# Kernel tuning notes

Hardware: AMD Instinct MI355X
Metric: run time of the kernel (lower is better)

The kernel has to match this reference:

```python
import jax, jax.numpy as jnp
import numpy as np

N = 11          # neighborhood size
HEADS = 4
DIM = 128
OUT_DIM = 128
HEAD_DIM = DIM // HEADS
LN_EPS = 1e-5


def unfold_neighborhood(x, n=N):
    # x: [B,H,W,C] -> [B,H,W,N,N,C]; matches torch F.unfold semantics:
    # out[b,h,w,i,j,c] = padded[b, h+i, w+j, c]
    B, H, W, C = x.shape
    P = (n - 1) // 2
    xp = jnp.pad(x, ((0, 0), (P, P), (P, P), (0, 0)))
    patches = jnp.stack(
        [xp[:, i:i + H, j:j + W, :] for i in range(n) for j in range(n)],
        axis=3)  # [B,H,W,N*N,C]
    return patches.reshape(B, H, W, n, n, C)


def setup_inputs() -> dict:
    key = jax.random.key(0)
    ks = jax.random.split(key, 6)
    B, H, W = 2, 64, 64
    q = jax.random.normal(ks[0], (B, H, W, DIM), dtype=jnp.float32)
    kv = jax.random.normal(ks[1], (B, H, W, DIM), dtype=jnp.float32)
    pos_enc = jax.random.normal(ks[2], (N, N, DIM), dtype=jnp.float32)
    # mlp: Linear(N*N*heads -> out_dim)
    fan_in = N * N * HEADS
    bound = 1.0 / np.sqrt(fan_in)
    mlp_w = jax.random.uniform(ks[3], (fan_in, OUT_DIM), jnp.float32, -bound, bound)
    mlp_b = jax.random.uniform(ks[4], (OUT_DIM,), jnp.float32, -bound, bound)
    ln_g = jnp.ones((OUT_DIM,), jnp.float32)
    ln_b = jnp.zeros((OUT_DIM,), jnp.float32)
    return {"q": q, "kv": kv, "pos_enc": pos_enc, "mlp_w": mlp_w,
            "mlp_b": mlp_b, "ln_g": ln_g, "ln_b": ln_b}


def reference(q, kv, pos_enc, mlp_w, mlp_b, ln_g, ln_b):
    B, H, W, C = q.shape
    kv_n = unfold_neighborhood(kv, N) + pos_enc            # [B,H,W,N,N,C]
    # faithful raw row-major reinterpretation of (N,N,C) -> (heads, N^2, head_dim)
    kv_mh = kv_n.reshape(B, H, W, HEADS, N * N, HEAD_DIM)
    q_mh = q.reshape(B, H, W, HEADS, HEAD_DIM)
    # per-pixel per-head dot products (note: original never applies scale)
    scores = jnp.einsum('bxyhnd,bxyhd->bxyhn', kv_mh, q_mh)
    scores = scores.reshape(B, H, W, HEADS * N * N)        # [B,H,W,484]
    mlp_out = jax.nn.gelu(scores @ mlp_w + mlp_b, approximate=False)
    # short_cut is Identity since dim == out_dim
    x = q + mlp_out
    mu = jnp.mean(x, axis=-1, keepdims=True)
    var = jnp.mean(jnp.square(x - mu), axis=-1, keepdims=True)
    return (x - mu) * jax.lax.rsqrt(var + LN_EPS) * ln_g + ln_b
```

## Files before the change

kernel.cpp:

```cpp
#include <hip/hip_runtime.h>
#include <math.h>

#define NB 11
#define PAD 5
#define DIM 128
#define NN 121
#define S_TOT 484
#define IMG 64
#define TILE 8
#define PDIM 74
#define SCP 520
#define PSCP 488
#define UCOLS 18
#define UCELLS 198
#define NT_KV 50
#define NT_POS 31
#define NPAD (2 * PDIM * PDIM)
#define KVB ((NPAD + 3) / 4)
#define LN_EPS 1e-5f

typedef __attribute__((ext_vector_type(8))) short bf16x8;
typedef __attribute__((ext_vector_type(4))) float f32x4;

static __device__ __forceinline__ unsigned short f2bf(float f) {
    unsigned u = __float_as_uint(f);
    u += 0x7FFF + ((u >> 16) & 1);
    return (unsigned short)(u >> 16);
}

__global__ __launch_bounds__(256) void prep_kernel(
    const float* __restrict__ kv, const float* __restrict__ w,
    const float* __restrict__ pos, unsigned short* __restrict__ pkvb,
    unsigned short* __restrict__ wfrag, unsigned short* __restrict__ posB)
{
    const int blk  = blockIdx.x;
    const int lane = threadIdx.x & 63;
    const int sub  = threadIdx.x >> 6;
    if (blk < KVB) {
        const int row = blk * 4 + sub;
        if (row < NPAD) {
            const int b  = row / (PDIM * PDIM);
            const int rr = row - b * PDIM * PDIM;
            const int py = rr / PDIM;
            const int px = rr - py * PDIM;
            const int ky = py - PAD, kx = px - PAD;
            unsigned v = 0;
            if ((unsigned)ky < (unsigned)IMG && (unsigned)kx < (unsigned)IMG) {
                const float2 f = *(const float2*)(kv + (((size_t)b * IMG + ky) * IMG + kx) * DIM + 2 * lane);
                v = (unsigned)f2bf(f.x) | ((unsigned)f2bf(f.y) << 16);
            }
            *(unsigned*)(pkvb + (size_t)row * DIM + 2 * lane) = v;
        }
    } else if (blk < KVB + 32) {
        const int idx = (blk - KVB) * 4 + sub;
        const int t   = idx & 15;
        const int n   = ((idx >> 4) << 4) + (lane & 15);
        const int kb  = t * 32 + ((lane >> 4) << 3);
        unsigned short v[8];
        #pragma unroll
        for (int j = 0; j < 8; ++j) {
            const int k = kb + j;
            v[j] = (k < S_TOT) ? f2bf(w[(size_t)k * DIM + n]) : (unsigned short)0;
        }
        *(uint4*)(wfrag + (((size_t)idx * 64 + lane) << 3)) = *(const uint4*)v;
    } else {
        const int nt = (blk - KVB - 32) * 4 + sub;
        if (nt < NT_POS) {
            const int m    = lane & 15, quad = lane >> 4;
            const int p    = 4 * nt + (m >> 2);
            const int r    = m & 3;
            unsigned short v[8];
            #pragma unroll
            for (int j = 0; j < 8; ++j)
                v[j] = (p <= 120) ? f2bf(pos[(size_t)p * DIM + 32 * r + 8 * quad + j])
                                  : (unsigned short)0;
            *(uint4*)(posB + (((size_t)nt * 64 + lane) << 3)) = *(const uint4*)v;
        }
    }
}

__global__ __launch_bounds__(512) void nca_kernel(
    const float* __restrict__ q, const unsigned short* __restrict__ pkvb,
    const unsigned short* __restrict__ posB, const unsigned short* __restrict__ wfrag,
    const float* __restrict__ bias, const float* __restrict__ gam,
    const float* __restrict__ bet, float* __restrict__ out)
{
    const int tile = blockIdx.x;
    const int pix0 = tile * TILE;
    const int x0 = pix0 & 63;
    const int y  = (pix0 >> 6) & 63;
    const int b  = pix0 >> 12;
    const int tid = threadIdx.x;

    __shared__ float qs[TILE][DIM];
    __shared__ float psc[TILE][PSCP];
    __shared__ __align__(16) unsigned short sc_bf[TILE][SCP];
    __shared__ float mlp[TILE][DIM];

    for (int i = tid; i < TILE * DIM; i += 512)
        qs[i >> 7][i & 127] = q[(size_t)pix0 * DIM + i];
    for (int i = tid; i < TILE * (SCP - S_TOT); i += 512)
        sc_bf[i / (SCP - S_TOT)][S_TOT + i % (SCP - S_TOT)] = 0;

    {
        const int wid  = tid >> 6;
        const int lane = tid & 63;
        const int n    = lane & 15, quad = lane >> 4;
        const int mt   = wid & 1;
        const int w4   = wid >> 1;
        const int pxl  = 4 * mt + quad;

        const float* qa = q + ((size_t)(pix0 + 4 * mt + (n >> 2))) * DIM
                            + 32 * (n & 3) + 8 * quad;
        const float4 fa0 = *(const float4*)qa;
        const float4 fa1 = *(const float4*)(qa + 4);
        unsigned short aq_[8] = {f2bf(fa0.x), f2bf(fa0.y), f2bf(fa0.z), f2bf(fa0.w),
                                 f2bf(fa1.x), f2bf(fa1.y), f2bf(fa1.z), f2bf(fa1.w)};
        const bf16x8 Aq = *(const bf16x8*)aq_;

        {
            const unsigned short* pb = posB + ((size_t)lane << 3);
            int nt = w4;
            bf16x8 Bc = *(const bf16x8*)(pb + (size_t)nt * 512);
            while (nt < NT_POS) {
                const int ntn = nt + 4;
                bf16x8 Bn = Bc;
                if (ntn < NT_POS) Bn = *(const bf16x8*)(pb + (size_t)ntn * 512);
                f32x4 acc = {0.f, 0.f, 0.f, 0.f};
                acc = __builtin_amdgcn_mfma_f32_16x16x32_bf16(Aq, Bc, acc, 0, 0, 0);
                const int s = 16 * nt + n;
                if (s < S_TOT) {
                    const int h = (271 * s) >> 15;
                    const float v = (h == 0) ? acc[0] : (h == 1) ? acc[1]
                                  : (h == 2) ? acc[2] : acc[3];
                    psc[pxl][s] = v;
                }
                Bc = Bn; nt = ntn;
            }
        }
        __syncthreads();

        {
            const int r  = n & 3;
            const int co = 32 * r + 8 * quad;
            const unsigned short* kvb = pkvb
                + ((size_t)((b * PDIM + y) * PDIM) + x0) * DIM + co;
            int c = 4 * w4 + (n >> 2);
            int i = 0, u = c;
            int nt = w4;
            bf16x8 Bc = *(const bf16x8*)(kvb + (size_t)(i * PDIM + u) * DIM);
            while (nt < NT_KV) {
                int cn = c + 16, in_ = i, un = u + 16;
                if (un >= UCOLS) { un -= UCOLS; ++in_; }
                if (cn > UCELLS - 1) { in_ = 10; un = UCOLS - 1; }
                bf16x8 Bn = Bc;
                if (nt + 4 < NT_KV)
                    Bn = *(const bf16x8*)(kvb + (size_t)(in_ * PDIM + un) * DIM);
                f32x4 acc = {0.f, 0.f, 0.f, 0.f};
                acc = __builtin_amdgcn_mfma_f32_16x16x32_bf16(Aq, Bc, acc, 0, 0, 0);
                const int jr = u - pxl;
                if ((unsigned)jr < 11u) {
                    const int s = 44 * i + 4 * jr + r;
                    const int h = (271 * s) >> 15;
                    const float v = ((h == 0) ? acc[0] : (h == 1) ? acc[1]
                                   : (h == 2) ? acc[2] : acc[3]) + psc[pxl][s];
                    sc_bf[pxl][s] = f2bf(v);
                }
                Bc = Bn; c = cn; i = in_; u = un; nt += 4;
            }
        }
    }
    __syncthreads();

    {
        const int wv   = tid >> 6;
        const int lane = tid & 63;
        const int m    = lane & 15;
        const int quad = lane >> 4;
        const unsigned short* bfr = wfrag + (((size_t)(wv * 16) * 64 + lane) << 3);
        const unsigned short* ap  = &sc_bf[m & 7][quad * 8];
        f32x4 acc = {0.f, 0.f, 0.f, 0.f};
        bf16x8 b0 = *(const bf16x8*)(bfr);
        bf16x8 b1 = *(const bf16x8*)(bfr + 512);
        bf16x8 b2 = *(const bf16x8*)(bfr + 1024);
        bf16x8 b3 = *(const bf16x8*)(bfr + 1536);
        #pragma unroll
        for (int t = 0; t < 16; ++t) {
            const bf16x8 a = *(const bf16x8*)(ap + t * 32);
            bf16x8 bn = b3;
            if (t + 4 < 16) bn = *(const bf16x8*)(bfr + (t + 4) * 512);
            acc = __builtin_amdgcn_mfma_f32_16x16x32_bf16(a, b0, acc, 0, 0, 0);
            b0 = b1; b1 = b2; b2 = b3; b3 = bn;
        }
        if (quad < 2) {
            #pragma unroll
            for (int reg = 0; reg < 4; ++reg)
                mlp[quad * 4 + reg][wv * 16 + m] = acc[reg];
        }
    }
    __syncthreads();

    for (int idx = tid; idx < TILE * DIM; idx += 512) {
        const int pix = idx >> 7, cc = idx & 127;
        const float v = mlp[pix][cc] + bias[cc];
        const float gl = 0.5f * v * (1.f + erff(v * 0.70710678118654752f));
        qs[pix][cc] += gl;
    }
    __syncthreads();

    {
        const int lane = tid & 63, wid = tid >> 6;
        const float v0 = qs[wid][lane], v1 = qs[wid][lane + 64];
        float sum = v0 + v1;
        #pragma unroll
        for (int off = 1; off < 64; off <<= 1) sum += __shfl_xor(sum, off, 64);
        const float mean = sum * (1.f / 128.f);
        const float d0 = v0 - mean, d1 = v1 - mean;
        float sq = d0 * d0 + d1 * d1;
        #pragma unroll
        for (int off = 1; off < 64; off <<= 1) sq += __shfl_xor(sq, off, 64);
        const float rstd = rsqrtf(sq * (1.f / 128.f) + LN_EPS);
        float* op = out + (size_t)(pix0 + wid) * DIM;
        op[lane]      = d0 * rstd * gam[lane]      + bet[lane];
        op[lane + 64] = d1 * rstd * gam[lane + 64] + bet[lane + 64];
    }
}

__global__ __launch_bounds__(512) void nca_kernel_nopad(
    const float* __restrict__ q, const float* __restrict__ kvsrc,
    const float* __restrict__ pos, const float* __restrict__ w,
    const float* __restrict__ bias, const float* __restrict__ gam,
    const float* __restrict__ bet, float* __restrict__ out)
{
    const int tile = blockIdx.x;
    const int pix0 = tile * TILE;
    const int x0 = pix0 & 63;
    const int y  = (pix0 >> 6) & 63;
    const int b  = pix0 >> 12;
    const int tid = threadIdx.x;

    __shared__ float qs[TILE][DIM];
    __shared__ float sc[S_TOT][TILE];
    __shared__ float part[4][TILE][DIM];

    for (int i = tid; i < TILE * DIM; i += 512)
        qs[i >> 7][i & 127] = q[(size_t)pix0 * DIM + i];
    __syncthreads();

    {
        const int pix = tid >> 6;
        const int grp = (tid >> 4) & 3;
        const int l16 = tid & 15;
        const int r   = l16 >> 2;
        const int dq  = 8 * (l16 & 3);
        const int ch  = 8 * l16;
        const int xpix = x0 + pix;
        int p = grp, i = 0, j = grp;
        int h = 0, rem = 4 * grp + r;
        const float* kvb  = kvsrc + (size_t)b * IMG * IMG * DIM + ch;
        const float* posb = pos + ch;
        float4 q0 = *(const float4*)(&qs[pix][dq]);
        float4 q1 = *(const float4*)(&qs[pix][dq + 4]);
        for (int it = 0; it < 31; ++it) {
            if (p <= 120) {
                float4 k0 = make_float4(0.f,0.f,0.f,0.f), k1 = k0;
                const int ky = y + i - PAD, kx = xpix + j - PAD;
                if (((unsigned)ky < (unsigned)IMG) && ((unsigned)kx < (unsigned)IMG)) {
                    const float* kp = kvb + (size_t)(ky * IMG + kx) * DIM;
                    k0 = *(const float4*)(kp);
                    k1 = *(const float4*)(kp + 4);
                }
                const float4 p0 = *(const float4*)(posb + (size_t)p * DIM);
                const float4 p1 = *(const float4*)(posb + (size_t)p * DIM + 4);
                float t = (k0.x + p0.x) * q0.x + (k0.y + p0.y) * q0.y
                        + (k0.z + p0.z) * q0.z + (k0.w + p0.w) * q0.w
                        + (k1.x + p1.x) * q1.x + (k1.y + p1.y) * q1.y
                        + (k1.z + p1.z) * q1.z + (k1.w + p1.w) * q1.w;
                t += __shfl_xor(t, 1, 64);
                t += __shfl_xor(t, 2, 64);
                if ((l16 & 3) == 0) sc[4 * p + r][pix] = t;
            }
            p += 4; j += 4;
            if (j >= NB) { j -= NB; ++i; }
            rem += 16;
            if (rem >= NN) {
                rem -= NN; ++h;
                q0 = *(const float4*)(&qs[pix][h * 32 + dq]);
                q1 = *(const float4*)(&qs[pix][h * 32 + dq + 4]);
            }
        }
    }
    __syncthreads();

    {
        const int l  = tid & 63;
        const int wv = tid >> 6;
        const int g  = wv >> 1;
        const int ph = wv & 1;
        const float* wc  = w + (size_t)(g * NN) * DIM + l;
        const float* scp = &sc[g * NN][ph * 4];
        float a00=0,a01=0,a10=0,a11=0,a20=0,a21=0,a30=0,a31=0;
        #pragma unroll 2
        for (int s = 0; s < NN; ++s) {
            const float4 sv = *(const float4*)(scp + s * 8);
            const float w0 = wc[(size_t)s * DIM];
            const float w1 = wc[(size_t)s * DIM + 64];
            a00 += sv.x * w0; a01 += sv.x * w1;
            a10 += sv.y * w0; a11 += sv.y * w1;
            a20 += sv.z * w0; a21 += sv.z * w1;
            a30 += sv.w * w0; a31 += sv.w * w1;
        }
        const int pb = ph * 4;
        part[g][pb+0][l] = a00; part[g][pb+0][l+64] = a01;
        part[g][pb+1][l] = a10; part[g][pb+1][l+64] = a11;
        part[g][pb+2][l] = a20; part[g][pb+2][l+64] = a21;
        part[g][pb+3][l] = a30; part[g][pb+3][l+64] = a31;
    }
    __syncthreads();

    for (int idx = tid; idx < TILE * DIM; idx += 512) {
        const int pix = idx >> 7, cc = idx & 127;
        float v = part[0][pix][cc] + part[1][pix][cc]
                + part[2][pix][cc] + part[3][pix][cc] + bias[cc];
        const float gl = 0.5f * v * (1.f + erff(v * 0.70710678118654752f));
        qs[pix][cc] += gl;
    }
    __syncthreads();

    {
        const int lane = tid & 63, wid = tid >> 6;
        const float v0 = qs[wid][lane], v1 = qs[wid][lane + 64];
        float sum = v0 + v1;
        #pragma unroll
        for (int off = 1; off < 64; off <<= 1) sum += __shfl_xor(sum, off, 64);
        const float mean = sum * (1.f / 128.f);
        const float d0 = v0 - mean, d1 = v1 - mean;
        float sq = d0 * d0 + d1 * d1;
        #pragma unroll
        for (int off = 1; off < 64; off <<= 1) sq += __shfl_xor(sq, off, 64);
        const float rstd = rsqrtf(sq * (1.f / 128.f) + LN_EPS);
        float* op = out + (size_t)(pix0 + wid) * DIM;
        op[lane]      = d0 * rstd * gam[lane]      + bet[lane];
        op[lane + 64] = d1 * rstd * gam[lane + 64] + bet[lane + 64];
    }
}

extern "C" void kernel_launch(void* const* d_in, const int* in_sizes, int n_in,
                              void* d_out, int out_size, void* d_ws, size_t ws_size,
                              hipStream_t stream) {
    const float* q    = (const float*)d_in[0];
    const float* kv   = (const float*)d_in[1];
    const float* pos  = (const float*)d_in[2];
    const float* w    = (const float*)d_in[3];
    const float* bias = (const float*)d_in[4];
    const float* gam  = (const float*)d_in[5];
    const float* bet  = (const float*)d_in[6];
    float* out = (float*)d_out;

    const int n_blocks = 2 * IMG * IMG / TILE;
    const size_t pkvb_bytes  = (size_t)2 * PDIM * PDIM * DIM * sizeof(unsigned short);
    const size_t wfrag_bytes = (size_t)8 * 16 * 64 * 8 * sizeof(unsigned short);
    const size_t posB_bytes  = (size_t)NT_POS * 64 * 8 * sizeof(unsigned short);

    if (ws_size >= pkvb_bytes + wfrag_bytes + posB_bytes) {
        unsigned short* pkvb  = (unsigned short*)d_ws;
        unsigned short* wfrag = (unsigned short*)((char*)d_ws + pkvb_bytes);
        unsigned short* posB  = (unsigned short*)((char*)d_ws + pkvb_bytes + wfrag_bytes);
        const int prep_blocks = KVB + 32 + (NT_POS + 3) / 4;
        prep_kernel<<<prep_blocks, 256, 0, stream>>>(kv, w, pos, pkvb, wfrag, posB);
        nca_kernel<<<n_blocks, 512, 0, stream>>>(q, pkvb, posB, wfrag, bias, gam, bet, out);
    } else {
        nca_kernel_nopad<<<n_blocks, 512, 0, stream>>>(q, kv, pos, w, bias, gam, bet, out);
    }
}
```

Measured before the change: 92.06 us.

## Drop padded bf16 kv prep pass; read fp32 kv directly with bounds checks

The prep kernel no longer builds a zero-padded bf16 copy of kv. The main kernel now loads fp32 kv straight from the input, bounds-checks each neighbour, and converts to bf16 in registers before the MFMA. Block indices are also swizzled so neighbouring tiles spread across the grid, probably for cache locality. This removes the prep pass and its write then re-read of kv, but doubles the bytes per neighbour load inside the hot loop and adds conversion ALU work.

After: 104.9 us. 13.9% more time.

```diff
diff --git a/kernel.cpp b/kernel.cpp
--- a/kernel.cpp
+++ b/kernel.cpp
@@ -8,15 +8,12 @@
 #define S_TOT 484
 #define IMG 64
 #define TILE 8
-#define PDIM 74
 #define SCP 520
 #define PSCP 488
 #define UCOLS 18
 #define UCELLS 198
 #define NT_KV 50
 #define NT_POS 31
-#define NPAD (2 * PDIM * PDIM)
-#define KVB ((NPAD + 3) / 4)
 #define LN_EPS 1e-5f
 
 typedef __attribute__((ext_vector_type(8))) short bf16x8;
@@ -29,30 +26,14 @@
 }
 
 __global__ __launch_bounds__(256) void prep_kernel(
-    const float* __restrict__ kv, const float* __restrict__ w,
-    const float* __restrict__ pos, unsigned short* __restrict__ pkvb,
+    const float* __restrict__ w, const float* __restrict__ pos,
     unsigned short* __restrict__ wfrag, unsigned short* __restrict__ posB)
 {
     const int blk  = blockIdx.x;
     const int lane = threadIdx.x & 63;
     const int sub  = threadIdx.x >> 6;
-    if (blk < KVB) {
-        const int row = blk * 4 + sub;
-        if (row < NPAD) {
-            const int b  = row / (PDIM * PDIM);
-            const int rr = row - b * PDIM * PDIM;
-            const int py = rr / PDIM;
-            const int px = rr - py * PDIM;
-            const int ky = py - PAD, kx = px - PAD;
-            unsigned v = 0;
-            if ((unsigned)ky < (unsigned)IMG && (unsigned)kx < (unsigned)IMG) {
-                const float2 f = *(const float2*)(kv + (((size_t)b * IMG + ky) * IMG + kx) * DIM + 2 * lane);
-                v = (unsigned)f2bf(f.x) | ((unsigned)f2bf(f.y) << 16);
-            }
-            *(unsigned*)(pkvb + (size_t)row * DIM + 2 * lane) = v;
-        }
-    } else if (blk < KVB + 32) {
-        const int idx = (blk - KVB) * 4 + sub;
+    if (blk < 32) {
+        const int idx = blk * 4 + sub;
         const int t   = idx & 15;
         const int n   = ((idx >> 4) << 4) + (lane & 15);
         const int kb  = t * 32 + ((lane >> 4) << 3);
@@ -64,7 +45,7 @@
         }
         *(uint4*)(wfrag + (((size_t)idx * 64 + lane) << 3)) = *(const uint4*)v;
     } else {
-        const int nt = (blk - KVB - 32) * 4 + sub;
+        const int nt = (blk - 32) * 4 + sub;
         if (nt < NT_POS) {
             const int m    = lane & 15, quad = lane >> 4;
             const int p    = 4 * nt + (m >> 2);
@@ -80,12 +61,13 @@
 }
 
 __global__ __launch_bounds__(512) void nca_kernel(
-    const float* __restrict__ q, const unsigned short* __restrict__ pkvb,
+    const float* __restrict__ q, const float* __restrict__ kv,
     const unsigned short* __restrict__ posB, const unsigned short* __restrict__ wfrag,
     const float* __restrict__ bias, const float* __restrict__ gam,
     const float* __restrict__ bet, float* __restrict__ out)
 {
-    const int tile = blockIdx.x;
+    const int g    = blockIdx.x;
+    const int tile = ((g & 7) << 7) | (g >> 3);
     const int pix0 = tile * TILE;
     const int x0 = pix0 & 63;
     const int y  = (pix0 >> 6) & 63;
@@ -143,19 +125,33 @@
         {
             const int r  = n & 3;
             const int co = 32 * r + 8 * quad;
-            const unsigned short* kvb = pkvb
-                + ((size_t)((b * PDIM + y) * PDIM) + x0) * DIM + co;
+            const float* kvb = kv + (size_t)b * IMG * IMG * DIM + co;
             int c = 4 * w4 + (n >> 2);
             int i = 0, u = c;
+            float4 k0 = make_float4(0.f, 0.f, 0.f, 0.f), k1 = k0;
+            {
+                const int ky = y + i - PAD, kx = x0 + u - PAD;
+                if ((unsigned)ky < (unsigned)IMG && (unsigned)kx < (unsigned)IMG) {
+                    const float* p = kvb + (size_t)(ky * IMG + kx) * DIM;
+                    k0 = *(const float4*)p; k1 = *(const float4*)(p + 4);
+                }
+            }
             int nt = w4;
-            bf16x8 Bc = *(const bf16x8*)(kvb + (size_t)(i * PDIM + u) * DIM);
             while (nt < NT_KV) {
                 int cn = c + 16, in_ = i, un = u + 16;
                 if (un >= UCOLS) { un -= UCOLS; ++in_; }
                 if (cn > UCELLS - 1) { in_ = 10; un = UCOLS - 1; }
-                bf16x8 Bn = Bc;
-                if (nt + 4 < NT_KV)
-                    Bn = *(const bf16x8*)(kvb + (size_t)(in_ * PDIM + un) * DIM);
+                float4 n0 = make_float4(0.f, 0.f, 0.f, 0.f), n1 = n0;
+                if (nt + 4 < NT_KV) {
+                    const int ky = y + in_ - PAD, kx = x0 + un - PAD;
+                    if ((unsigned)ky < (unsigned)IMG && (unsigned)kx < (unsigned)IMG) {
+                        const float* p = kvb + (size_t)(ky * IMG + kx) * DIM;
+                        n0 = *(const float4*)p; n1 = *(const float4*)(p + 4);
+                    }
+                }
+                unsigned short bv[8] = {f2bf(k0.x), f2bf(k0.y), f2bf(k0.z), f2bf(k0.w),
+                                        f2bf(k1.x), f2bf(k1.y), f2bf(k1.z), f2bf(k1.w)};
+                const bf16x8 Bc = *(const bf16x8*)bv;
                 f32x4 acc = {0.f, 0.f, 0.f, 0.f};
                 acc = __builtin_amdgcn_mfma_f32_16x16x32_bf16(Aq, Bc, acc, 0, 0, 0);
                 const int jr = u - pxl;
@@ -166,7 +162,7 @@
                                    : (h == 2) ? acc[2] : acc[3]) + psc[pxl][s];
                     sc_bf[pxl][s] = f2bf(v);
                 }
-                Bc = Bn; c = cn; i = in_; u = un; nt += 4;
+                k0 = n0; k1 = n1; c = cn; i = in_; u = un; nt += 4;
             }
         }
     }
@@ -358,17 +354,14 @@
     float* out = (float*)d_out;
 
     const int n_blocks = 2 * IMG * IMG / TILE;
-    const size_t pkvb_bytes  = (size_t)2 * PDIM * PDIM * DIM * sizeof(unsigned short);
     const size_t wfrag_bytes = (size_t)8 * 16 * 64 * 8 * sizeof(unsigned short);
     const size_t posB_bytes  = (size_t)NT_POS * 64 * 8 * sizeof(unsigned short);
 
-    if (ws_size >= pkvb_bytes + wfrag_bytes + posB_bytes) {
-        unsigned short* pkvb  = (unsigned short*)d_ws;
-        unsigned short* wfrag = (unsigned short*)((char*)d_ws + pkvb_bytes);
-        unsigned short* posB  = (unsigned short*)((char*)d_ws + pkvb_bytes + wfrag_bytes);
-        const int prep_blocks = KVB + 32 + (NT_POS + 3) / 4;
-        prep_kernel<<<prep_blocks, 256, 0, stream>>>(kv, w, pos, pkvb, wfrag, posB);
-        nca_kernel<<<n_blocks, 512, 0, stream>>>(q, pkvb, posB, wfrag, bias, gam, bet, out);
+    if (ws_size >= wfrag_bytes + posB_bytes) {
+        unsigned short* wfrag = (unsigned short*)d_ws;
+        unsigned short* posB  = (unsigned short*)((char*)d_ws + wfrag_bytes);
+        prep_kernel<<<40, 256, 0, stream>>>(w, pos, wfrag, posB);
+        nca_kernel<<<n_blocks, 512, 0, stream>>>(q, kv, posB, wfrag, bias, gam, bet, out);
     } else {
         nca_kernel_nopad<<<n_blocks, 512, 0, stream>>>(q, kv, pos, w, bias, gam, bet, out);
     }
```
